# Optimization experiments

Measured on AMD Instinct MI355X. Metric: run time of the kernel, lower is better.

## Reference

```python
import jax, jax.numpy as jnp
import numpy as np


def setup_inputs() -> dict:
    key = jax.random.key(0)
    k1, k2, k3 = jax.random.split(key, 3)
    B, S, E = 4, 8192, 1024
    x = jax.random.normal(k1, (B, S, E), dtype=jnp.float32)
    # torch nn.Linear weights have shape [out_features, in_features]
    W1 = jax.random.normal(k2, (3 * E, E), dtype=jnp.float32) * (1.0 / np.sqrt(E))
    W2 = jax.random.normal(k3, (E, E), dtype=jnp.float32) * (1.0 / np.sqrt(E))
    return {"x": x, "W1": W1, "W2": W2, "heads": 16}


def reference(x, W1, W2, heads):
    B, S, E = x.shape
    h = heads
    e = E // h
    # qkv projection: [B,S,3E] -> 'b s (n h e) -> n b h s e'
    qkv = (x @ W1.T).reshape(B, S, 3, h, e)
    qkv = jnp.transpose(qkv, (2, 0, 3, 1, 4))  # [3,B,h,S,e]
    q, k, v = qkv[0], qkv[1], qkv[2]
    # score: [B,h,e,e], softmax over last dim (c)
    score = jax.nn.softmax(jnp.einsum('bhnk,bhnc->bhkc', k / 4, v), axis=-1)
    # einsum 'bhnk,bhkc->bhnk': elementwise over k, sum over c
    attn = jax.nn.softmax(jnp.einsum('bhnk,bhkc->bhnk', q / 4, score), axis=-1)
    # 'b h s e -> b s (h e)' then linear_2
    out = jnp.transpose(attn, (0, 2, 1, 3)).reshape(B, S, E) @ W2.T
    return out
```

## Files before the change

### kernel.cpp

```cpp
#include <hip/hip_runtime.h>
#include <hip/hip_bf16.h>
#include <stdint.h>

static constexpr int MTOT = 32768;
static constexpr int KD   = 1024;
static constexpr int ND   = 1024;

static constexpr int BM = 256, BN = 256, BK = 64;
static constexpr int NT = KD / BK;
static constexpr int BUF_BYTES = 65536;
static constexpr int BOFF = 32768;
static constexpr int HALF = 16384;

typedef __bf16 bf16x8 __attribute__((ext_vector_type(8)));
typedef float  f32x4  __attribute__((ext_vector_type(4)));

__device__ __forceinline__ unsigned short f2bf_rne(float f) {
  union { float f; uint32_t u; } c; c.f = f;
  uint32_t u = c.u;
  return (unsigned short)((u + 0x7fffu + ((u >> 16) & 1u)) >> 16);
}

__global__ void cast_all(const float* __restrict__ x,
                         const float* __restrict__ W1,
                         const float* __restrict__ W2,
                         unsigned short* __restrict__ xb,
                         unsigned short* __restrict__ w1b,
                         unsigned short* __restrict__ w2b) {
  constexpr int n4x = MTOT * KD / 4;
  constexpr int n4w = KD * KD / 4;
  constexpr int total = n4x + 2 * n4w;
  int idx = blockIdx.x * blockDim.x + threadIdx.x;
  int stride = gridDim.x * blockDim.x;
  for (int i = idx; i < total; i += stride) {
    const float* s; unsigned short* d; int j;
    if (i < n4x)            { s = x;  d = xb;  j = i; }
    else if (i < n4x + n4w) { s = W1; d = w1b; j = i - n4x; }
    else                    { s = W2; d = w2b; j = i - n4x - n4w; }
    float4 v = reinterpret_cast<const float4*>(s)[j];
    ushort4 o;
    o.x = f2bf_rne(v.x); o.y = f2bf_rne(v.y);
    o.z = f2bf_rne(v.z); o.w = f2bf_rne(v.w);
    reinterpret_cast<ushort4*>(d)[j] = o;
  }
}

__device__ __forceinline__ void gload_lds16(const void* g, void* lds) {
  __builtin_amdgcn_global_load_lds(
      (const __attribute__((address_space(1))) unsigned int*)g,
      (__attribute__((address_space(3))) unsigned int*)lds, 16, 0, 0);
}

template <int SOFTMAX>
__global__ __launch_bounds__(512, 2)
void gemm8(const unsigned short* __restrict__ A,
           const unsigned short* __restrict__ Bm,
           void* __restrict__ Cout) {
  extern __shared__ __align__(16) char ldsc[];

  const int tid  = threadIdx.x;
  const int lane = tid & 63;
  const int wid  = tid >> 6;
  const int wm = wid >> 2, wn = wid & 3;
  const int fr = lane & 15, fq = lane >> 4;

  const int bid0 = blockIdx.x;
  const int bid  = ((bid0 & 7) << 6) | (bid0 >> 3);
  const int brow = (bid >> 2) * BM;
  const int bcol = (bid & 3) * BN;

  const int srow  = tid >> 3;
  const int sslot = (tid & 7) ^ (srow & 7);
  const unsigned short* gA = A  + (size_t)(brow + srow) * KD + sslot * 8;
  const unsigned short* gB = Bm + (size_t)(bcol + srow) * KD + sslot * 8;

  f32x4  acc[8][4] = {};
  bf16x8 a0[4][2], a1[4][2], bA[2][2], bB[2][2];

  auto STAGE = [&](const unsigned short* g, int h, int kt, int b, int opOff) {
    const unsigned short* gu = g + (size_t)(h * 128) * KD + kt * BK;
    char* du = ldsc + b * BUF_BYTES + opOff + h * HALF + (wid << 10);
    gload_lds16(gu, du);
    gload_lds16(gu + (size_t)64 * KD, du + 8192);
  };

  auto rdA = [&](int b, bf16x8 (*dst)[2], int mBase) {
    const char* base = ldsc + b * BUF_BYTES + wm * HALF;
    #pragma unroll
    for (int mm = 0; mm < 4; ++mm) {
      const int r = (mBase + mm) * 16 + fr;
      #pragma unroll
      for (int ks = 0; ks < 2; ++ks)
        dst[mm][ks] = *(const bf16x8*)(base + (r << 7) +
                        ((ks * 64 + fq * 16) ^ ((r & 7) << 4)));
    }
  };
  auto rdB = [&](int b, int nBase, bf16x8 (*dst)[2]) {
    const char* base = ldsc + b * BUF_BYTES + BOFF + (wn >> 1) * HALF;
    #pragma unroll
    for (int nn = 0; nn < 2; ++nn) {
      const int r = (wn & 1) * 64 + (nBase + nn) * 16 + fr;
      #pragma unroll
      for (int ks = 0; ks < 2; ++ks)
        dst[nn][ks] = *(const bf16x8*)(base + (r << 7) +
                       ((ks * 64 + fq * 16) ^ ((r & 7) << 4)));
    }
  };
  auto MFMA16 = [&](int mBase, int nBase, bf16x8 (*af)[2], bf16x8 (*bf)[2]) {
    __builtin_amdgcn_s_setprio(1);
    #pragma unroll
    for (int ks = 0; ks < 2; ++ks)
      #pragma unroll
      for (int mm = 0; mm < 4; ++mm)
        #pragma unroll
        for (int nn = 0; nn < 2; ++nn)
          acc[mBase + mm][nBase + nn] = __builtin_amdgcn_mfma_f32_16x16x32_bf16(
              af[mm][ks], bf[nn][ks], acc[mBase + mm][nBase + nn], 0, 0, 0);
    __builtin_amdgcn_s_setprio(0);
  };

  auto tileStep = [&](int T, int cur, int nxt) {
    const int tp1 = (T + 1 < NT) ? T + 1 : NT - 1;
    const int tp2 = (T + 2 < NT) ? T + 2 : NT - 1;

    rdA(cur, a0, 0);
    STAGE(gB, 0, tp1, nxt, BOFF);
    MFMA16(0, 0, a0, bA);

    rdA(cur, a1, 4);
    STAGE(gB, 1, tp1, nxt, BOFF);
    MFMA16(4, 0, a1, bA);
    __builtin_amdgcn_s_barrier();

    rdB(cur, 2, bB);
    STAGE(gA, 0, tp2, cur, 0);
    MFMA16(4, 2, a1, bB);

    STAGE(gA, 1, tp2, cur, 0);
    asm volatile("s_waitcnt vmcnt(4)" ::: "memory");
    __builtin_amdgcn_s_barrier();
    rdB(nxt, 0, bA);
    MFMA16(0, 2, a0, bB);
    __builtin_amdgcn_s_barrier();
  };

  STAGE(gA, 0, 0, 0, 0);    STAGE(gA, 1, 0, 0, 0);
  STAGE(gB, 0, 0, 0, BOFF); STAGE(gB, 1, 0, 0, BOFF);
  STAGE(gA, 0, 1, 1, 0);    STAGE(gA, 1, 1, 1, 0);
  asm volatile("s_waitcnt vmcnt(4)" ::: "memory");
  __builtin_amdgcn_s_barrier();
  rdB(0, 0, bA);

  for (int T = 0; T < NT; T += 2) {
    tileStep(T,     0, 1);
    tileStep(T + 1, 1, 0);
  }

  if constexpr (SOFTMAX) {
    unsigned short* attn = reinterpret_cast<unsigned short*>(Cout);
    constexpr float CEXP = 0.25f * 1.44269504088896340736f;
    #pragma unroll
    for (int m = 0; m < 8; ++m) {
      const int row = brow + wm * 128 + m * 16 + fq * 4;
      #pragma unroll
      for (int j = 0; j < 4; ++j) {
        float v0 = acc[m][0][j], v1 = acc[m][1][j];
        float v2 = acc[m][2][j], v3 = acc[m][3][j];
        float mx = fmaxf(fmaxf(v0, v1), fmaxf(v2, v3));
        #pragma unroll
        for (int s = 1; s < 16; s <<= 1) mx = fmaxf(mx, __shfl_xor(mx, s, 64));
        float p0 = exp2f((v0 - mx) * CEXP);
        float p1 = exp2f((v1 - mx) * CEXP);
        float p2 = exp2f((v2 - mx) * CEXP);
        float p3 = exp2f((v3 - mx) * CEXP);
        float sm = p0 + p1 + p2 + p3;
        #pragma unroll
        for (int s = 1; s < 16; s <<= 1) sm += __shfl_xor(sm, s, 64);
        const float inv = 1.0f / sm;
        unsigned short* dst =
            attn + (size_t)(row + j) * ND + (bcol + wn * 64 + fr);
        dst[0]  = f2bf_rne(p0 * inv);
        dst[16] = f2bf_rne(p1 * inv);
        dst[32] = f2bf_rne(p2 * inv);
        dst[48] = f2bf_rne(p3 * inv);
      }
    }
  } else {
    float* Cf = reinterpret_cast<float*>(Cout);
    char* wlds = ldsc + wid * 16384;
    #pragma unroll
    for (int h = 0; h < 2; ++h) {
      asm volatile("" ::: "memory");
      #pragma unroll
      for (int mm = 0; mm < 4; ++mm)
        #pragma unroll
        for (int n = 0; n < 4; ++n)
          #pragma unroll
          for (int j = 0; j < 4; ++j)
            *(float*)(wlds + (((mm * 16 + fq * 4 + j) << 6) + n * 16 + fr) * 4)
                = acc[4 * h + mm][n][j];
      asm volatile("s_waitcnt lgkmcnt(0)" ::: "memory");
      const int rbase = brow + wm * 128 + h * 64;
      #pragma unroll
      for (int i = 0; i < 16; ++i) {
        const int idx16 = i * 64 + lane;
        const int rl = idx16 >> 4;
        const int c4 = (idx16 & 15) << 2;
        f32x4 v = *(const f32x4*)(wlds + (size_t)idx16 * 16);
        *(f32x4*)(&Cf[(size_t)(rbase + rl) * ND + (bcol + wn * 64 + c4)]) = v;
      }
      asm volatile("s_waitcnt lgkmcnt(0)" ::: "memory");
    }
  }
}

extern "C" void kernel_launch(void* const* d_in, const int* in_sizes, int n_in,
                              void* d_out, int out_size, void* d_ws, size_t ws_size,
                              hipStream_t stream) {
  const float* x  = (const float*)d_in[0];
  const float* W1 = (const float*)d_in[1];
  const float* W2 = (const float*)d_in[2];
  float* out = (float*)d_out;

  char* ws = (char*)d_ws;
  unsigned short* xb   = (unsigned short*)(ws);
  unsigned short* w1b  = (unsigned short*)(ws + (size_t)67108864);
  unsigned short* w2b  = (unsigned short*)(ws + (size_t)69206016);
  unsigned short* attn = (unsigned short*)(ws + (size_t)71303168);

  hipFuncSetAttribute(reinterpret_cast<const void*>(gemm8<1>),
                      hipFuncAttributeMaxDynamicSharedMemorySize, 131072);
  hipFuncSetAttribute(reinterpret_cast<const void*>(gemm8<0>),
                      hipFuncAttributeMaxDynamicSharedMemorySize, 131072);

  cast_all<<<2048, 256, 0, stream>>>(x, W1, W2, xb, w1b, w2b);

  const int nblk = (MTOT / BM) * (ND / BN);
  gemm8<1><<<nblk, 512, 131072, stream>>>(xb, w1b, (void*)attn);
  gemm8<0><<<nblk, 512, 131072, stream>>>(attn, w2b, (void*)out);
}
```

Measured before the change: 185.4 us.

## Replace LDS-staged GEMM main loop with direct global-to-register fragment loads

Drops the global_load_lds double-buffered LDS staging, the swizzled LDS reads and the barriers in both GEMM kernels. Each wave now loads its MFMA A and B fragments straight from global memory into registers, prefetching one K-tile ahead. The projection GEMM launches with no dynamic LDS. This removes LDS traffic and block-wide synchronisation, but every wave now fetches its own copy of shared A and B rows, so global and cache traffic rise several-fold. Latency hiding also depends only on register prefetch with uncoalesced 16-byte row segments.

```diff
diff --git a/kernel.cpp b/kernel.cpp
--- a/kernel.cpp
+++ b/kernel.cpp
@@ -8,9 +8,6 @@
 
 static constexpr int BM = 256, BN = 256, BK = 64;
 static constexpr int NT = KD / BK;
-static constexpr int BUF_BYTES = 65536;
-static constexpr int BOFF = 32768;
-static constexpr int HALF = 16384;
 
 typedef __bf16 bf16x8 __attribute__((ext_vector_type(8)));
 typedef float  f32x4  __attribute__((ext_vector_type(4)));
@@ -45,12 +42,6 @@
   }
 }
 
-__device__ __forceinline__ void gload_lds16(const void* g, void* lds) {
-  __builtin_amdgcn_global_load_lds(
-      (const __attribute__((address_space(1))) unsigned int*)g,
-      (__attribute__((address_space(3))) unsigned int*)lds, 16, 0, 0);
-}
-
 template <int SOFTMAX>
 __global__ __launch_bounds__(512, 2)
 void gemm8(const unsigned short* __restrict__ A,
@@ -69,42 +60,30 @@
   const int brow = (bid >> 2) * BM;
   const int bcol = (bid & 3) * BN;
 
-  const int srow  = tid >> 3;
-  const int sslot = (tid & 7) ^ (srow & 7);
-  const unsigned short* gA = A  + (size_t)(brow + srow) * KD + sslot * 8;
-  const unsigned short* gB = Bm + (size_t)(bcol + srow) * KD + sslot * 8;
+  const int sRow = __builtin_amdgcn_readfirstlane(brow + wm * 128);
+  const int sCol = __builtin_amdgcn_readfirstlane(bcol + wn * 64);
+  const unsigned short* Abase = A  + (size_t)sRow * KD;
+  const unsigned short* Bbase = Bm + (size_t)sCol * KD;
+
+  const int lt = fr * KD + fq * 8;
+  int voff = lt;
 
   f32x4  acc[8][4] = {};
-  bf16x8 a0[4][2], a1[4][2], bA[2][2], bB[2][2];
-
-  auto STAGE = [&](const unsigned short* g, int h, int kt, int b, int opOff) {
-    const unsigned short* gu = g + (size_t)(h * 128) * KD + kt * BK;
-    char* du = ldsc + b * BUF_BYTES + opOff + h * HALF + (wid << 10);
-    gload_lds16(gu, du);
-    gload_lds16(gu + (size_t)64 * KD, du + 8192);
+  bf16x8 a0[4][2], a1[4][2], b01A[2][2], b01B[2][2], b23[2][2];
+
+  auto loadA = [&](bf16x8 (*dst)[2], int mBase, int v) {
+    #pragma unroll
+    for (int mm = 0; mm < 4; ++mm)
+      #pragma unroll
+      for (int ks = 0; ks < 2; ++ks)
+        dst[mm][ks] = *(const bf16x8*)(Abase + (mBase + mm) * 16 * KD + v + ks * 32);
   };
-
-  auto rdA = [&](int b, bf16x8 (*dst)[2], int mBase) {
-    const char* base = ldsc + b * BUF_BYTES + wm * HALF;
-    #pragma unroll
-    for (int mm = 0; mm < 4; ++mm) {
-      const int r = (mBase + mm) * 16 + fr;
+  auto loadB = [&](bf16x8 (*dst)[2], int nBase, int v) {
+    #pragma unroll
+    for (int nn = 0; nn < 2; ++nn)
       #pragma unroll
       for (int ks = 0; ks < 2; ++ks)
-        dst[mm][ks] = *(const bf16x8*)(base + (r << 7) +
-                        ((ks * 64 + fq * 16) ^ ((r & 7) << 4)));
-    }
-  };
-  auto rdB = [&](int b, int nBase, bf16x8 (*dst)[2]) {
-    const char* base = ldsc + b * BUF_BYTES + BOFF + (wn >> 1) * HALF;
-    #pragma unroll
-    for (int nn = 0; nn < 2; ++nn) {
-      const int r = (wn & 1) * 64 + (nBase + nn) * 16 + fr;
-      #pragma unroll
-      for (int ks = 0; ks < 2; ++ks)
-        dst[nn][ks] = *(const bf16x8*)(base + (r << 7) +
-                       ((ks * 64 + fq * 16) ^ ((r & 7) << 4)));
-    }
+        dst[nn][ks] = *(const bf16x8*)(Bbase + (nBase + nn) * 16 * KD + v + ks * 32);
   };
   auto MFMA16 = [&](int mBase, int nBase, bf16x8 (*af)[2], bf16x8 (*bf)[2]) {
     __builtin_amdgcn_s_setprio(1);
@@ -119,42 +98,26 @@
     __builtin_amdgcn_s_setprio(0);
   };
 
-  auto tileStep = [&](int T, int cur, int nxt) {
-    const int tp1 = (T + 1 < NT) ? T + 1 : NT - 1;
-    const int tp2 = (T + 2 < NT) ? T + 2 : NT - 1;
-
-    rdA(cur, a0, 0);
-    STAGE(gB, 0, tp1, nxt, BOFF);
-    MFMA16(0, 0, a0, bA);
-
-    rdA(cur, a1, 4);
-    STAGE(gB, 1, tp1, nxt, BOFF);
-    MFMA16(4, 0, a1, bA);
-    __builtin_amdgcn_s_barrier();
-
-    rdB(cur, 2, bB);
-    STAGE(gA, 0, tp2, cur, 0);
-    MFMA16(4, 2, a1, bB);
-
-    STAGE(gA, 1, tp2, cur, 0);
-    asm volatile("s_waitcnt vmcnt(4)" ::: "memory");
-    __builtin_amdgcn_s_barrier();
-    rdB(nxt, 0, bA);
-    MFMA16(0, 2, a0, bB);
-    __builtin_amdgcn_s_barrier();
-  };
-
-  STAGE(gA, 0, 0, 0, 0);    STAGE(gA, 1, 0, 0, 0);
-  STAGE(gB, 0, 0, 0, BOFF); STAGE(gB, 1, 0, 0, BOFF);
-  STAGE(gA, 0, 1, 1, 0);    STAGE(gA, 1, 1, 1, 0);
-  asm volatile("s_waitcnt vmcnt(4)" ::: "memory");
-  __builtin_amdgcn_s_barrier();
-  rdB(0, 0, bA);
+#define TSTEP(B01C, B01N)                                                   \
+  loadA(a1, 4, voff);                               \
+  loadB(B01N, 0, voff + BK);                    \
+  MFMA16(0, 0, a0, B01C);                                           \
+  MFMA16(0, 2, a0, b23);                                   \
+  loadA(a0, 0, voff + BK);                   \
+  MFMA16(4, 2, a1, b23);                                  \
+  loadB(b23, 2, voff + BK);                     \
+  MFMA16(4, 0, a1, B01C);                                           \
+  voff += BK;
+
+  loadA(a0, 0, voff);
+  loadB(b01A, 0, voff);
+  loadB(b23, 2, voff);
 
   for (int T = 0; T < NT; T += 2) {
-    tileStep(T,     0, 1);
-    tileStep(T + 1, 1, 0);
+    TSTEP(b01A, b01B)
+    TSTEP(b01B, b01A)
   }
+#undef TSTEP
 
   if constexpr (SOFTMAX) {
     unsigned short* attn = reinterpret_cast<unsigned short*>(Cout);
@@ -228,14 +191,12 @@
   unsigned short* w2b  = (unsigned short*)(ws + (size_t)69206016);
   unsigned short* attn = (unsigned short*)(ws + (size_t)71303168);
 
-  hipFuncSetAttribute(reinterpret_cast<const void*>(gemm8<1>),
-                      hipFuncAttributeMaxDynamicSharedMemorySize, 131072);
   hipFuncSetAttribute(reinterpret_cast<const void*>(gemm8<0>),
                       hipFuncAttributeMaxDynamicSharedMemorySize, 131072);
 
   cast_all<<<2048, 256, 0, stream>>>(x, W1, W2, xb, w1b, w2b);
 
   const int nblk = (MTOT / BM) * (ND / BN);
-  gemm8<1><<<nblk, 512, 131072, stream>>>(xb, w1b, (void*)attn);
+  gemm8<1><<<nblk, 512, 0, stream>>>(xb, w1b, (void*)attn);
   gemm8<0><<<nblk, 512, 131072, stream>>>(attn, w2b, (void*)out);
 }
```

Result: slower. 451.8 us (+143.8%).
